# Performance work log

Hardware: AMD Instinct MI355X
Metric: run time of the kernel (lower is better)

Reference implementation:

```python
import jax, jax.numpy as jnp
import numpy as np

D = 128

def setup_inputs() -> dict:
    key = jax.random.key(0)
    k1, k2, k3, k4, k5, k6, k7 = jax.random.split(key, 7)
    B, L = 2048, 200
    target = jax.random.normal(k1, (B, D), dtype=jnp.float32)
    item_seq = jax.random.normal(k2, (B, L, D), dtype=jnp.float32)
    seq_len = jax.random.randint(k3, (B,), 0, 200, dtype=jnp.int64 if jax.config.jax_enable_x64 else jnp.int32)
    # MLP params: Linear(4D -> 2D), Linear(2D -> 1), PyTorch-style init scale
    s1 = 1.0 / np.sqrt(4 * D)
    s2 = 1.0 / np.sqrt(2 * D)
    W1 = jax.random.uniform(k4, (4 * D, 2 * D), minval=-s1, maxval=s1, dtype=jnp.float32)
    b1 = jax.random.uniform(k5, (2 * D,), minval=-s1, maxval=s1, dtype=jnp.float32)
    W2 = jax.random.uniform(k6, (2 * D, 1), minval=-s2, maxval=s2, dtype=jnp.float32)
    b2 = jax.random.uniform(k7, (1,), minval=-s2, maxval=s2, dtype=jnp.float32)
    return {"target": target, "item_seq": item_seq, "seq_len": seq_len,
            "W1": W1, "b1": b1, "W2": W2, "b2": b2}

def reference(target, item_seq, seq_len, W1, b1, W2, b2):
    B, L, Dd = item_seq.shape
    t = target[:, None, :]                              # B 1 D (broadcast over L)
    tgt = jnp.broadcast_to(t, (B, L, Dd))
    sub = item_seq - tgt
    dot = item_seq * tgt
    mlp_in = jnp.concatenate([tgt, item_seq, sub, dot], axis=-1)   # B L 4D
    h = jax.nn.relu(jnp.einsum('blf,fh->blh', mlp_in, W1) + b1)    # B L 2D
    score = jnp.einsum('blh,ho->blo', h, W2) + b2                  # B L 1
    mask = (jnp.arange(L)[None, :] < seq_len[:, None]).astype(item_seq.dtype)  # B L
    weighted = score * item_seq * mask[:, :, None]                 # B L D
    return jnp.sum(weighted, axis=1)                               # B D
```

## Files before the change

kernel.cpp:

```cpp
#include <hip/hip_runtime.h>
#include <hip/hip_bf16.h>

typedef short short8 __attribute__((ext_vector_type(8)));
typedef float f32x4 __attribute__((ext_vector_type(4)));

#define XSTRIDE 264

static __device__ inline short f2bf(float f) {
    unsigned u = __float_as_uint(f);
    unsigned r = (u + 0x7fffu + ((u >> 16) & 1u)) >> 16;
    return (short)r;
}
static __device__ inline float bf2f(short s) {
    return __uint_as_float(((unsigned)(unsigned short)s) << 16);
}

__global__ void make_wu(const float* __restrict__ W1, float* __restrict__ Wu) {
    int idx = blockIdx.x * 256 + threadIdx.x;
    Wu[idx] = W1[idx] - W1[idx + 256 * 256];
}

__global__ void repack_w(const float* __restrict__ W1, short* __restrict__ Wfrag) {
    int idx = blockIdx.x * 256 + threadIdx.x;
    int j = idx & 7;
    int l = (idx >> 3) & 63;
    int s = (idx >> 9) & 7;
    int t = idx >> 12;
    int k = s * 32 + ((l >> 4) << 3) + j;
    int n = t * 16 + (l & 15);
    float v;
    if (k < 128) v = W1[(128 + k) * 256 + n] + W1[(256 + k) * 256 + n];
    else         v = W1[(384 + (k - 128)) * 256 + n];
    Wfrag[idx] = f2bf(v);
}

__launch_bounds__(256, 2)
__global__ void din_main(const float* __restrict__ target, const float* __restrict__ item_seq,
                         const int* __restrict__ seq_len, const float* __restrict__ W2,
                         const float* __restrict__ b2p, const short* __restrict__ Wfrag,
                         const float* __restrict__ Wu, const float* __restrict__ b1,
                         float* __restrict__ out) {
    const int b = blockIdx.x;
    const int tid = threadIdx.x;
    const int lane = tid & 63;
    const int wave = tid >> 6;
    const int col = lane & 15;
    const int q = lane >> 4;

    __shared__ __attribute__((aligned(16))) short Xl[16 * XSTRIDE];
    __shared__ __attribute__((aligned(16))) float tshared[128];
    __shared__ float u_s[256];
    __shared__ float w2_s[256];
    __shared__ float scoreP[4][16];
    __shared__ float out_s[128];

    const int slen = seq_len[b];
    const int ntiles = (slen + 15) >> 4;
    const float b2 = b2p[0];

    const int r = tid >> 4;
    const int c = (tid & 15) << 3;

    float4 v0, v1;
    if (ntiles > 0) {
        int lr = r;
        const float4* src = (const float4*)(item_seq + (((size_t)b * 200 + lr) * 128 + c));
        v0 = src[0]; v1 = src[1];
    }

    if (tid < 128) tshared[tid] = target[b * 128 + tid];
    w2_s[tid] = W2[tid];
    __syncthreads();

    {
        float uacc = b1[tid];
#pragma unroll 8
        for (int d = 0; d < 128; ++d) uacc += tshared[d] * Wu[d * 256 + tid];
        u_s[tid] = uacc;
    }

    float tgt8[8];
    {
        const float4* t4 = (const float4*)(tshared + c);
        float4 ta = t4[0], tb = t4[1];
        tgt8[0] = ta.x; tgt8[1] = ta.y; tgt8[2] = ta.z; tgt8[3] = ta.w;
        tgt8[4] = tb.x; tgt8[5] = tb.y; tgt8[6] = tb.z; tgt8[7] = tb.w;
    }

    short8 bfrag[4][8];
    {
        const short* base = Wfrag + ((size_t)(wave * 32) * 64 + lane) * 8;
#pragma unroll
        for (int i = 0; i < 4; i++)
#pragma unroll
            for (int s = 0; s < 8; s++)
                bfrag[i][s] = *(const short8*)(base + (size_t)((i * 8 + s) * 64) * 8);
    }

    float out_val = 0.f;
    f32x4 acc[4];

    for (int mt = 0; mt < ntiles; ++mt) {
        const int l0 = mt * 16;
        __syncthreads();

        {
            float v[8] = {v0.x, v0.y, v0.z, v0.w, v1.x, v1.y, v1.z, v1.w};
            short8 p0, p1;
#pragma unroll
            for (int i = 0; i < 8; i++) {
                p0[i] = f2bf(v[i]);
                p1[i] = f2bf(v[i] * tgt8[i]);
            }
            short* xr = Xl + r * XSTRIDE;
            *(short8*)(xr + c) = p0;
            *(short8*)(xr + 128 + c) = p1;
        }
        __syncthreads();

        if (mt + 1 < ntiles) {
            int lr = l0 + 16 + r;
            if (lr > 199) lr = 199;
            const float4* src = (const float4*)(item_seq + (((size_t)b * 200 + lr) * 128 + c));
            v0 = src[0]; v1 = src[1];
        }

#pragma unroll
        for (int i = 0; i < 4; i++) acc[i] = (f32x4){0.f, 0.f, 0.f, 0.f};

        const short* arow = Xl + col * XSTRIDE + q * 8;
#pragma unroll
        for (int s = 0; s < 8; s++) {
            short8 afrag = *(const short8*)(arow + s * 32);
#pragma unroll
            for (int i = 0; i < 4; i++)
                acc[i] = __builtin_amdgcn_mfma_f32_16x16x32_bf16(afrag, bfrag[i][s], acc[i], 0, 0, 0);
        }

        float sv[4] = {0.f, 0.f, 0.f, 0.f};
#pragma unroll
        for (int i = 0; i < 4; i++) {
            int j = (wave * 4 + i) * 16 + col;
            float uj = u_s[j], wj = w2_s[j];
#pragma unroll
            for (int rg = 0; rg < 4; rg++) {
                float h = acc[i][rg] + uj;
                h = h > 0.f ? h : 0.f;
                sv[rg] += h * wj;
            }
        }
#pragma unroll
        for (int off = 1; off < 16; off <<= 1) {
#pragma unroll
            for (int rg = 0; rg < 4; rg++) sv[rg] += __shfl_xor(sv[rg], off, 64);
        }
        if (col == 0) {
#pragma unroll
            for (int rg = 0; rg < 4; rg++) scoreP[wave][q * 4 + rg] = sv[rg];
        }
        __syncthreads();

        {
            int d = tid & 127;
            int mbase = (tid >> 7) * 8;
#pragma unroll
            for (int mm = 0; mm < 8; mm++) {
                int m = mbase + mm;
                int l = l0 + m;
                float s = scoreP[0][m] + scoreP[1][m] + scoreP[2][m] + scoreP[3][m] + b2;
                s = (l < slen) ? s : 0.f;
                out_val += s * bf2f(Xl[m * XSTRIDE + d]);
            }
        }
    }

    __syncthreads();
    if (tid >= 128) out_s[tid - 128] = out_val;
    __syncthreads();
    if (tid < 128) out[b * 128 + tid] = out_val + out_s[tid];
}

extern "C" void kernel_launch(void* const* d_in, const int* in_sizes, int n_in,
                              void* d_out, int out_size, void* d_ws, size_t ws_size,
                              hipStream_t stream) {
    const float* target   = (const float*)d_in[0];
    const float* item_seq = (const float*)d_in[1];
    const int*   seq_len  = (const int*)d_in[2];
    const float* W1       = (const float*)d_in[3];
    const float* b1       = (const float*)d_in[4];
    const float* W2       = (const float*)d_in[5];
    const float* b2       = (const float*)d_in[6];
    float* out = (float*)d_out;

    char* ws = (char*)d_ws;
    float* Wu    = (float*)ws;
    short* Wfrag = (short*)(ws + 131072);

    make_wu<<<128, 256, 0, stream>>>(W1, Wu);
    repack_w<<<256, 256, 0, stream>>>(W1, Wfrag);
    din_main<<<2048, 256, 0, stream>>>(target, item_seq, seq_len, W2, b2, Wfrag, Wu, b1, out);
}
```

Baseline: 334.8 us.

## Split each batch row across two blocks with atomic output accumulation

Each batch row's sequence tiles are now split between two blocks, with partial sums combined through atomicAdd into an output zeroed by a merged prep kernel. The two weight-prep kernels become one launch, and launch bounds rise to four blocks per SM. The goal is more parallelism and better load balance across uneven sequence lengths. In exchange, each half-block repeats the u-vector matvec and the B-fragment loads, and the higher occupancy target may cause register spills given the large bfrag array.

```diff
diff --git a/kernel.cpp b/kernel.cpp
--- a/kernel.cpp
+++ b/kernel.cpp
@@ -15,37 +15,49 @@
     return __uint_as_float(((unsigned)(unsigned short)s) << 16);
 }
 
-__global__ void make_wu(const float* __restrict__ W1, float* __restrict__ Wu) {
+__global__ void prep(const float* __restrict__ W1, float* __restrict__ Wu,
+                     short* __restrict__ Wfrag, float* __restrict__ out) {
     int idx = blockIdx.x * 256 + threadIdx.x;
-    Wu[idx] = W1[idx] - W1[idx + 256 * 256];
-}
-
-__global__ void repack_w(const float* __restrict__ W1, short* __restrict__ Wfrag) {
-    int idx = blockIdx.x * 256 + threadIdx.x;
-    int j = idx & 7;
-    int l = (idx >> 3) & 63;
-    int s = (idx >> 9) & 7;
-    int t = idx >> 12;
-    int k = s * 32 + ((l >> 4) << 3) + j;
-    int n = t * 16 + (l & 15);
-    float v;
-    if (k < 128) v = W1[(128 + k) * 256 + n] + W1[(256 + k) * 256 + n];
-    else         v = W1[(384 + (k - 128)) * 256 + n];
-    Wfrag[idx] = f2bf(v);
-}
-
-__launch_bounds__(256, 2)
+    if (idx < 32768) {
+        Wu[idx] = W1[idx] - W1[idx + 256 * 256];
+    } else if (idx < 98304) {
+        int i = idx - 32768;
+        int j = i & 7;
+        int l = (i >> 3) & 63;
+        int s = (i >> 9) & 7;
+        int t = i >> 12;
+        int k = s * 32 + ((l >> 4) << 3) + j;
+        int n = t * 16 + (l & 15);
+        float v;
+        if (k < 128) v = W1[(128 + k) * 256 + n] + W1[(256 + k) * 256 + n];
+        else         v = W1[(384 + (k - 128)) * 256 + n];
+        Wfrag[i] = f2bf(v);
+    } else {
+        out[idx - 98304] = 0.f;
+    }
+}
+
+__launch_bounds__(256, 4)
 __global__ void din_main(const float* __restrict__ target, const float* __restrict__ item_seq,
                          const int* __restrict__ seq_len, const float* __restrict__ W2,
                          const float* __restrict__ b2p, const short* __restrict__ Wfrag,
                          const float* __restrict__ Wu, const float* __restrict__ b1,
                          float* __restrict__ out) {
-    const int b = blockIdx.x;
+    const int bid = blockIdx.x;
+    const int b = bid >> 1;
+    const int half = bid & 1;
     const int tid = threadIdx.x;
     const int lane = tid & 63;
     const int wave = tid >> 6;
     const int col = lane & 15;
     const int q = lane >> 4;
+
+    const int slen = seq_len[b];
+    const int nt = (slen + 15) >> 4;
+    const int h0 = (nt + 1) >> 1;
+    const int t0 = half ? h0 : 0;
+    const int t1 = half ? nt : h0;
+    if (t0 >= t1) return;
 
     __shared__ __attribute__((aligned(16))) short Xl[16 * XSTRIDE];
     __shared__ __attribute__((aligned(16))) float tshared[128];
@@ -54,16 +66,15 @@
     __shared__ float scoreP[4][16];
     __shared__ float out_s[128];
 
-    const int slen = seq_len[b];
-    const int ntiles = (slen + 15) >> 4;
     const float b2 = b2p[0];
 
     const int r = tid >> 4;
     const int c = (tid & 15) << 3;
 
     float4 v0, v1;
-    if (ntiles > 0) {
-        int lr = r;
+    {
+        int lr = t0 * 16 + r;
+        if (lr > 199) lr = 199;
         const float4* src = (const float4*)(item_seq + (((size_t)b * 200 + lr) * 128 + c));
         v0 = src[0]; v1 = src[1];
     }
@@ -100,7 +111,7 @@
     float out_val = 0.f;
     f32x4 acc[4];
 
-    for (int mt = 0; mt < ntiles; ++mt) {
+    for (int mt = t0; mt < t1; ++mt) {
         const int l0 = mt * 16;
         __syncthreads();
 
@@ -118,7 +129,7 @@
         }
         __syncthreads();
 
-        if (mt + 1 < ntiles) {
+        if (mt + 1 < t1) {
             int lr = l0 + 16 + r;
             if (lr > 199) lr = 199;
             const float4* src = (const float4*)(item_seq + (((size_t)b * 200 + lr) * 128 + c));
@@ -177,7 +188,7 @@
     __syncthreads();
     if (tid >= 128) out_s[tid - 128] = out_val;
     __syncthreads();
-    if (tid < 128) out[b * 128 + tid] = out_val + out_s[tid];
+    if (tid < 128) atomicAdd(&out[b * 128 + tid], out_val + out_s[tid]);
 }
 
 extern "C" void kernel_launch(void* const* d_in, const int* in_sizes, int n_in,
@@ -196,7 +207,6 @@
     float* Wu    = (float*)ws;
     short* Wfrag = (short*)(ws + 131072);
 
-    make_wu<<<128, 256, 0, stream>>>(W1, Wu);
-    repack_w<<<256, 256, 0, stream>>>(W1, Wfrag);
-    din_main<<<2048, 256, 0, stream>>>(target, item_seq, seq_len, W2, b2, Wfrag, Wu, b1, out);
-}
+    prep<<<1408, 256, 0, stream>>>(W1, Wu, Wfrag, out);
+    din_main<<<4096, 256, 0, stream>>>(target, item_seq, seq_len, W2, b2, Wfrag, Wu, b1, out);
+}
```

New measurement: 521.1 us. +55.6%, slower.

## Fold target into per-batch weights to halve MFMA K and batch U computation

Applied to the files above, without the earlier changes.

The dot-product term item*target is folded into the weight matrix: each block builds its own bf16 B fragments as Wbc + target_k*Wd, which shrinks the GEMM K dimension from 256 to 128 and the LDS tile to one half. The u = target*Wu + b1 projection moves to a separate kernel that processes 8 batches per block, so W1 reads are shared across batches. The X tile is also double-buffered, which drops one barrier per tile, and the score partials are laid out so they can be read as a float4. In exchange, each block pays per-batch weight-fragment construction in its prologue, and rounding the combined weight to bf16 adds a small precision change.

```diff
diff --git a/kernel.cpp b/kernel.cpp
--- a/kernel.cpp
+++ b/kernel.cpp
@@ -4,7 +4,7 @@
 typedef short short8 __attribute__((ext_vector_type(8)));
 typedef float f32x4 __attribute__((ext_vector_type(4)));
 
-#define XSTRIDE 264
+#define XS 136
 
 static __device__ inline short f2bf(float f) {
     unsigned u = __float_as_uint(f);
@@ -15,110 +15,124 @@
     return __uint_as_float(((unsigned)(unsigned short)s) << 16);
 }
 
-__global__ void make_wu(const float* __restrict__ W1, float* __restrict__ Wu) {
+__global__ void prep(const float* __restrict__ W1, short* __restrict__ Wbc,
+                     short* __restrict__ Wd) {
     int idx = blockIdx.x * 256 + threadIdx.x;
-    Wu[idx] = W1[idx] - W1[idx + 256 * 256];
-}
-
-__global__ void repack_w(const float* __restrict__ W1, short* __restrict__ Wfrag) {
-    int idx = blockIdx.x * 256 + threadIdx.x;
-    int j = idx & 7;
-    int l = (idx >> 3) & 63;
-    int s = (idx >> 9) & 7;
-    int t = idx >> 12;
+    int half = idx >> 15;
+    int i = idx & 32767;
+    int j = i & 7;
+    int l = (i >> 3) & 63;
+    int s = (i >> 9) & 3;
+    int t = i >> 11;
     int k = s * 32 + ((l >> 4) << 3) + j;
     int n = t * 16 + (l & 15);
-    float v;
-    if (k < 128) v = W1[(128 + k) * 256 + n] + W1[(256 + k) * 256 + n];
-    else         v = W1[(384 + (k - 128)) * 256 + n];
-    Wfrag[idx] = f2bf(v);
+    if (half == 0) Wbc[i] = f2bf(W1[(128 + k) * 256 + n] + W1[(256 + k) * 256 + n]);
+    else           Wd[i]  = f2bf(W1[(384 + k) * 256 + n]);
+}
+
+__global__ void compute_u(const float* __restrict__ target, const float* __restrict__ W1,
+                          const float* __restrict__ b1, float* __restrict__ U) {
+    const int b8 = blockIdx.x;
+    const int tid = threadIdx.x;
+    __shared__ float tl[1024];
+#pragma unroll
+    for (int k = 0; k < 4; k++) tl[k * 256 + tid] = target[b8 * 1024 + k * 256 + tid];
+    __syncthreads();
+    float acc[8] = {0.f, 0.f, 0.f, 0.f, 0.f, 0.f, 0.f, 0.f};
+#pragma unroll 8
+    for (int d = 0; d < 128; ++d) {
+        float wud = W1[d * 256 + tid] - W1[(256 + d) * 256 + tid];
+#pragma unroll
+        for (int r = 0; r < 8; r++) acc[r] += tl[r * 128 + d] * wud;
+    }
+    float bj = b1[tid];
+#pragma unroll
+    for (int r = 0; r < 8; r++) U[(b8 * 8 + r) * 256 + tid] = acc[r] + bj;
 }
 
 __launch_bounds__(256, 2)
 __global__ void din_main(const float* __restrict__ target, const float* __restrict__ item_seq,
                          const int* __restrict__ seq_len, const float* __restrict__ W2,
-                         const float* __restrict__ b2p, const short* __restrict__ Wfrag,
-                         const float* __restrict__ Wu, const float* __restrict__ b1,
+                         const float* __restrict__ b2p, const short* __restrict__ Wbc,
+                         const short* __restrict__ Wd, const float* __restrict__ U,
                          float* __restrict__ out) {
     const int b = blockIdx.x;
     const int tid = threadIdx.x;
     const int lane = tid & 63;
-    const int wave = tid >> 6;
+    const int w = tid >> 6;
     const int col = lane & 15;
     const int q = lane >> 4;
 
-    __shared__ __attribute__((aligned(16))) short Xl[16 * XSTRIDE];
-    __shared__ __attribute__((aligned(16))) float tshared[128];
+    const int slen = seq_len[b];
+    const int nt = (slen + 15) >> 4;
+
+    __shared__ __attribute__((aligned(16))) short Xl[2][16 * XS];
+    __shared__ __attribute__((aligned(16))) float tsh[128];
     __shared__ float u_s[256];
     __shared__ float w2_s[256];
-    __shared__ float scoreP[4][16];
+    __shared__ __attribute__((aligned(16))) float scoreP[16][4];
     __shared__ float out_s[128];
-
-    const int slen = seq_len[b];
-    const int ntiles = (slen + 15) >> 4;
-    const float b2 = b2p[0];
 
     const int r = tid >> 4;
     const int c = (tid & 15) << 3;
 
     float4 v0, v1;
-    if (ntiles > 0) {
-        int lr = r;
-        const float4* src = (const float4*)(item_seq + (((size_t)b * 200 + lr) * 128 + c));
+    {
+        const float4* src = (const float4*)(item_seq + (((size_t)b * 200 + r) * 128 + c));
         v0 = src[0]; v1 = src[1];
     }
 
-    if (tid < 128) tshared[tid] = target[b * 128 + tid];
+    if (tid < 128) tsh[tid] = target[b * 128 + tid];
+    u_s[tid] = U[b * 256 + tid];
     w2_s[tid] = W2[tid];
-    __syncthreads();
-
-    {
-        float uacc = b1[tid];
-#pragma unroll 8
-        for (int d = 0; d < 128; ++d) uacc += tshared[d] * Wu[d * 256 + tid];
-        u_s[tid] = uacc;
-    }
-
-    float tgt8[8];
-    {
-        const float4* t4 = (const float4*)(tshared + c);
-        float4 ta = t4[0], tb = t4[1];
-        tgt8[0] = ta.x; tgt8[1] = ta.y; tgt8[2] = ta.z; tgt8[3] = ta.w;
-        tgt8[4] = tb.x; tgt8[5] = tb.y; tgt8[6] = tb.z; tgt8[7] = tb.w;
-    }
-
-    short8 bfrag[4][8];
-    {
-        const short* base = Wfrag + ((size_t)(wave * 32) * 64 + lane) * 8;
-#pragma unroll
-        for (int i = 0; i < 4; i++)
-#pragma unroll
-            for (int s = 0; s < 8; s++)
-                bfrag[i][s] = *(const short8*)(base + (size_t)((i * 8 + s) * 64) * 8);
-    }
-
+    const float b2 = b2p[0];
+    __syncthreads();
+
+    short8 bfrag[4][4];
+#pragma unroll
+    for (int s = 0; s < 4; s++) {
+        const float4* tp = (const float4*)(tsh + s * 32 + q * 8);
+        float4 ta = tp[0], tb = tp[1];
+        float tk[8] = {ta.x, ta.y, ta.z, ta.w, tb.x, tb.y, tb.z, tb.w};
+#pragma unroll
+        for (int i = 0; i < 4; i++) {
+            size_t off = ((size_t)((w * 4 + i) * 4 + s) * 64 + lane) * 8;
+            short8 bc = *(const short8*)(Wbc + off);
+            short8 dd = *(const short8*)(Wd + off);
+            short8 e;
+#pragma unroll
+            for (int j = 0; j < 8; j++) e[j] = f2bf(bf2f(bc[j]) + tk[j] * bf2f(dd[j]));
+            bfrag[i][s] = e;
+        }
+    }
+
+    float u_c[4], w2c[4];
+#pragma unroll
+    for (int i = 0; i < 4; i++) {
+        int j = (w * 4 + i) * 16 + col;
+        u_c[i] = u_s[j];
+        w2c[i] = w2_s[j];
+    }
+
+    const int d = tid & 127;
+    const int g = tid >> 7;
     float out_val = 0.f;
     f32x4 acc[4];
 
-    for (int mt = 0; mt < ntiles; ++mt) {
+    for (int mt = 0; mt < nt; ++mt) {
         const int l0 = mt * 16;
-        __syncthreads();
+        short* xb = Xl[mt & 1];
 
         {
             float v[8] = {v0.x, v0.y, v0.z, v0.w, v1.x, v1.y, v1.z, v1.w};
-            short8 p0, p1;
-#pragma unroll
-            for (int i = 0; i < 8; i++) {
-                p0[i] = f2bf(v[i]);
-                p1[i] = f2bf(v[i] * tgt8[i]);
-            }
-            short* xr = Xl + r * XSTRIDE;
-            *(short8*)(xr + c) = p0;
-            *(short8*)(xr + 128 + c) = p1;
+            short8 p;
+#pragma unroll
+            for (int j = 0; j < 8; j++) p[j] = f2bf(v[j]);
+            *(short8*)(xb + r * XS + c) = p;
         }
         __syncthreads();
 
-        if (mt + 1 < ntiles) {
+        if (mt + 1 < nt) {
             int lr = l0 + 16 + r;
             if (lr > 199) lr = 199;
             const float4* src = (const float4*)(item_seq + (((size_t)b * 200 + lr) * 128 + c));
@@ -127,27 +141,26 @@
 
 #pragma unroll
         for (int i = 0; i < 4; i++) acc[i] = (f32x4){0.f, 0.f, 0.f, 0.f};
-
-        const short* arow = Xl + col * XSTRIDE + q * 8;
-#pragma unroll
-        for (int s = 0; s < 8; s++) {
-            short8 afrag = *(const short8*)(arow + s * 32);
+        const short* arow = xb + col * XS + q * 8;
+#pragma unroll
+        for (int s = 0; s < 4; s++) {
+            short8 af = *(const short8*)(arow + s * 32);
 #pragma unroll
             for (int i = 0; i < 4; i++)
-                acc[i] = __builtin_amdgcn_mfma_f32_16x16x32_bf16(afrag, bfrag[i][s], acc[i], 0, 0, 0);
-        }
-
-        float sv[4] = {0.f, 0.f, 0.f, 0.f};
-#pragma unroll
-        for (int i = 0; i < 4; i++) {
-            int j = (wave * 4 + i) * 16 + col;
-            float uj = u_s[j], wj = w2_s[j];
-#pragma unroll
-            for (int rg = 0; rg < 4; rg++) {
-                float h = acc[i][rg] + uj;
+                acc[i] = __builtin_amdgcn_mfma_f32_16x16x32_bf16(af, bfrag[i][s], acc[i], 0, 0, 0);
+        }
+
+        float sv[4];
+#pragma unroll
+        for (int rg = 0; rg < 4; rg++) {
+            float s0 = 0.f;
+#pragma unroll
+            for (int i = 0; i < 4; i++) {
+                float h = acc[i][rg] + u_c[i];
                 h = h > 0.f ? h : 0.f;
-                sv[rg] += h * wj;
+                s0 += h * w2c[i];
             }
+            sv[rg] = s0;
         }
 #pragma unroll
         for (int off = 1; off < 16; off <<= 1) {
@@ -156,28 +169,25 @@
         }
         if (col == 0) {
 #pragma unroll
-            for (int rg = 0; rg < 4; rg++) scoreP[wave][q * 4 + rg] = sv[rg];
+            for (int rg = 0; rg < 4; rg++) scoreP[q * 4 + rg][w] = sv[rg];
         }
         __syncthreads();
 
-        {
-            int d = tid & 127;
-            int mbase = (tid >> 7) * 8;
-#pragma unroll
-            for (int mm = 0; mm < 8; mm++) {
-                int m = mbase + mm;
-                int l = l0 + m;
-                float s = scoreP[0][m] + scoreP[1][m] + scoreP[2][m] + scoreP[3][m] + b2;
-                s = (l < slen) ? s : 0.f;
-                out_val += s * bf2f(Xl[m * XSTRIDE + d]);
-            }
-        }
-    }
-
-    __syncthreads();
-    if (tid >= 128) out_s[tid - 128] = out_val;
-    __syncthreads();
-    if (tid < 128) out[b * 128 + tid] = out_val + out_s[tid];
+#pragma unroll
+        for (int mm = 0; mm < 8; mm++) {
+            int m = g * 8 + mm;
+            int l = l0 + m;
+            float4 sp = *(const float4*)&scoreP[m][0];
+            float s = (sp.x + sp.y) + (sp.z + sp.w) + b2;
+            s = (l < slen) ? s : 0.f;
+            out_val += s * bf2f(xb[m * XS + d]);
+        }
+    }
+
+    __syncthreads();
+    if (g == 1) out_s[d] = out_val;
+    __syncthreads();
+    if (g == 0) out[b * 128 + d] = out_val + out_s[d];
 }
 
 extern "C" void kernel_launch(void* const* d_in, const int* in_sizes, int n_in,
@@ -193,10 +203,11 @@
     float* out = (float*)d_out;
 
     char* ws = (char*)d_ws;
-    float* Wu    = (float*)ws;
-    short* Wfrag = (short*)(ws + 131072);
-
-    make_wu<<<128, 256, 0, stream>>>(W1, Wu);
-    repack_w<<<256, 256, 0, stream>>>(W1, Wfrag);
-    din_main<<<2048, 256, 0, stream>>>(target, item_seq, seq_len, W2, b2, Wfrag, Wu, b1, out);
-}
+    short* Wbc = (short*)ws;
+    short* Wd  = (short*)(ws + 65536);
+    float* U   = (float*)(ws + 131072);
+
+    prep<<<256, 256, 0, stream>>>(W1, Wbc, Wd);
+    compute_u<<<256, 256, 0, stream>>>(target, W1, b1, U);
+    din_main<<<2048, 256, 0, stream>>>(target, item_seq, seq_len, W2, b2, Wbc, Wd, U, out);
+}
```

After: 312.3 us. 1.07x faster.
